# Performance work log

Hardware: AMD Instinct MI355X
Metric: run time of the kernel (lower is better)

Reference implementation:

```python
import jax, jax.numpy as jnp
import numpy as np

N = 10000
E = 160000
D_IN = 512
D_OUT = 512


def setup_inputs() -> dict:
    key = jax.random.key(0)
    k1, k2, k3, k4, k5 = jax.random.split(key, 5)
    x = jax.random.normal(k1, (N, D_IN), dtype=jnp.float32)
    edge_index = jax.random.randint(k2, (2, E), 0, N, dtype=jnp.int64)
    edge_attr = jax.random.uniform(k3, (E,), dtype=jnp.float32)
    W = jax.random.normal(k4, (D_IN, D_OUT), dtype=jnp.float32) * 0.05
    b = jax.random.normal(k5, (D_OUT,), dtype=jnp.float32) * 0.05
    return {"x": x, "edge_index": edge_index, "edge_attr": edge_attr, "W": W, "b": b}


def reference(x, edge_index, edge_attr, W, b):
    # PyG GCNConv with normalize=True, add_self_loops=True, edge_weight=edge_attr.
    n = x.shape[0]
    row, col = edge_index[0], edge_index[1]
    # Add self loops with weight 1.0 (fill_value=1.)
    loop = jnp.arange(n, dtype=edge_index.dtype)
    row_f = jnp.concatenate([row, loop])      # [E+N] source nodes
    col_f = jnp.concatenate([col, loop])      # [E+N] target nodes
    ew = jnp.concatenate([edge_attr, jnp.ones((n,), dtype=edge_attr.dtype)])
    # Symmetric normalization: deg computed over target index (col)
    deg = jax.ops.segment_sum(ew, col_f, num_segments=n)
    dinv = jnp.where(deg > 0, jax.lax.rsqrt(deg), 0.0)
    norm = dinv[row_f] * ew * dinv[col_f]     # [E+N]
    # Linear transform (no bias inside lin), then gather-scale-scatter
    h = x @ W                                  # [N, D_OUT]
    msg = h[row_f] * norm[:, None]             # [E+N, D_OUT]
    out = jax.ops.segment_sum(msg, col_f, num_segments=n)
    return out + b
```

## Files before the change

### kernel.cpp

```cpp
#include <hip/hip_runtime.h>

#define NN 10000
#define EE 160000
#define DD 512
#define CAP 128

typedef float floatx4 __attribute__((ext_vector_type(4)));
typedef short short8 __attribute__((ext_vector_type(8)));

#define AS3(p) ((__attribute__((address_space(3))) void*)(p))
#define AS1(p) ((const __attribute__((address_space(1))) void*)(p))

static __device__ __forceinline__ unsigned short f2bf(float f) {
    unsigned int u = __float_as_uint(f);
    unsigned int r = (u + 0x7fffu + ((u >> 16) & 1u)) >> 16;
    return (unsigned short)r;
}
static __device__ __forceinline__ float bflo(unsigned int u) {
    return __uint_as_float(u << 16);
}
static __device__ __forceinline__ float bfhi(unsigned int u) {
    return __uint_as_float(u & 0xffff0000u);
}


#define XB_BLOCKS 5000
#define WT_BLOCKS 256
#define EDGE_BLOCKS 625

__global__ __launch_bounds__(256) void k_prep(const float* __restrict__ x,
                                              const float* __restrict__ W,
                                              const int* __restrict__ row,
                                              const int* __restrict__ col,
                                              const float* __restrict__ ew,
                                              unsigned short* __restrict__ xb,
                                              unsigned short* __restrict__ wtb,
                                              float* __restrict__ deg,
                                              int* __restrict__ cursor,
                                              uint2* __restrict__ erw) {
    const int b = blockIdx.x;
    const int tid = threadIdx.x;
    if (b < XB_BLOCKS) {
        int gid = b * 256 + tid;
        float4 v = *(const float4*)&x[(size_t)gid * 4];
        unsigned int p0 = (unsigned int)f2bf(v.x) | ((unsigned int)f2bf(v.y) << 16);
        unsigned int p1 = (unsigned int)f2bf(v.z) | ((unsigned int)f2bf(v.w) << 16);
        *(uint2*)&xb[(size_t)gid * 4] = make_uint2(p0, p1);
    } else if (b < XB_BLOCKS + WT_BLOCKS) {
        __shared__ float T[32][33];
        int idx = b - XB_BLOCKS;
        int bi = idx & 15;
        int bj = idx >> 4;
        int r0 = tid >> 5;
        int cc = tid & 31;
        #pragma unroll
        for (int k = 0; k < 4; k++) {
            int r = r0 + k * 8;
            T[r][cc] = W[(size_t)(bi * 32 + r) * DD + bj * 32 + cc];
        }
        __syncthreads();
        #pragma unroll
        for (int k = 0; k < 4; k++) {
            int r = r0 + k * 8;
            wtb[(size_t)(bj * 32 + r) * DD + bi * 32 + cc] = f2bf(T[cc][r]);
        }
    } else {
        int e = (b - XB_BLOCKS - WT_BLOCKS) * 256 + tid;
        int r = row[e];
        int t = col[e];
        float w = ew[e];
        atomicAdd(&deg[t], w);
        int p = atomicAdd(&cursor[t], 1);
        if (p < CAP) erw[t * CAP + p] = make_uint2((unsigned int)r, __float_as_uint(w));
    }
}


__global__ __launch_bounds__(256) void k_gemm_mfma(const unsigned short* __restrict__ xb,
                                                   const unsigned short* __restrict__ wtb,
                                                   const float* __restrict__ deg,
                                                   unsigned short* __restrict__ hb) {
    __shared__ unsigned short As[64 * 32];
    __shared__ unsigned short Bs[128 * 32];

    const int tid = threadIdx.x;
    const int wave = tid >> 6;
    const int lane = tid & 63;

    const int bm = blockIdx.x * 64;
    const int bn = blockIdx.y * 128;

    const int wm = (wave >> 1) * 32;
    const int wn = (wave & 1) * 64;

    const int fm = lane & 15;
    const int kb = (lane >> 4) * 8;

    floatx4 acc[2][4];
    #pragma unroll
    for (int i = 0; i < 2; i++)
        #pragma unroll
        for (int j = 0; j < 4; j++)
            acc[i][j] = (floatx4){0.f, 0.f, 0.f, 0.f};

    const int srow = lane >> 2;
    const int scol = (lane & 3) * 8;

    for (int k0 = 0; k0 < DD; k0 += 32) {
        {
            int r = wave * 16 + srow;
            int gr = bm + r; if (gr > NN - 1) gr = NN - 1;
            __builtin_amdgcn_global_load_lds(AS1(xb + (size_t)gr * DD + k0 + scol),
                                             AS3(&As[wave * 512]), 16, 0, 0);
        }
        #pragma unroll
        for (int cc = 0; cc < 2; cc++) {
            int c = wave + cc * 4;
            int nr = bn + c * 16 + srow;
            __builtin_amdgcn_global_load_lds(AS1(wtb + (size_t)nr * DD + k0 + scol),
                                             AS3(&Bs[c * 512]), 16, 0, 0);
        }
        __syncthreads();

        short8 af[2], bfr[4];
        #pragma unroll
        for (int mi = 0; mi < 2; mi++)
            af[mi] = *(const short8*)&As[(wm + mi * 16 + fm) * 32 + kb];
        #pragma unroll
        for (int ni = 0; ni < 4; ni++)
            bfr[ni] = *(const short8*)&Bs[(wn + ni * 16 + fm) * 32 + kb];

        #pragma unroll
        for (int mi = 0; mi < 2; mi++)
            #pragma unroll
            for (int ni = 0; ni < 4; ni++)
                acc[mi][ni] = __builtin_amdgcn_mfma_f32_16x16x32_bf16(af[mi], bfr[ni], acc[mi][ni], 0, 0, 0);

        __syncthreads();
    }

    float dv[2][4];
    #pragma unroll
    for (int mi = 0; mi < 2; mi++) {
        int rbase = bm + wm + mi * 16 + (lane >> 4) * 4;
        #pragma unroll
        for (int j = 0; j < 4; j++) {
            int rg = rbase + j; if (rg > NN - 1) rg = NN - 1;
            dv[mi][j] = rsqrtf(deg[rg] + 1.0f);
        }
    }

    #pragma unroll
    for (int mi = 0; mi < 2; mi++) {
        #pragma unroll
        for (int ni = 0; ni < 4; ni++) {
            int colg = bn + wn + ni * 16 + (lane & 15);
            int rbase = bm + wm + mi * 16 + (lane >> 4) * 4;
            #pragma unroll
            for (int j = 0; j < 4; j++) {
                int rg = rbase + j;
                if (rg < NN) hb[(size_t)rg * DD + colg] = f2bf(acc[mi][ni][j] * dv[mi][j]);
            }
        }
    }
}


#define EDGE_FMA2(P, W) \
    acc[0] += bflo(P.x) * W; acc[1] += bfhi(P.x) * W; \
    acc[2] += bflo(P.y) * W; acc[3] += bfhi(P.y) * W;

__global__ __launch_bounds__(128, 8) void k_aggregate(const int* __restrict__ cursor,
                                                      const uint2* __restrict__ erw,
                                                      const unsigned short* __restrict__ hb,
                                                      const float* __restrict__ deg,
                                                      const float* __restrict__ bias,
                                                      float* __restrict__ out) {
    const int h = threadIdx.x >> 6;
    const int t = threadIdx.x & 63;
    const int bid = blockIdx.x;
    const int half = bid & 1;
    const int i = (bid >> 1) * 2 + h;
    const int c = half * 256 + t * 4;

    __shared__ int   s_r[2][CAP];
    __shared__ float s_w[2][CAP];

    int cnt = cursor[i];
    if (cnt > CAP) cnt = CAP;
    const uint2* bkt = erw + (size_t)i * CAP;
    if (t < cnt)      { uint2 p = bkt[t];      s_r[h][t]      = (int)p.x; s_w[h][t]      = __uint_as_float(p.y); }
    if (t + 64 < cnt) { uint2 p = bkt[t + 64]; s_r[h][t + 64] = (int)p.x; s_w[h][t + 64] = __uint_as_float(p.y); }

    float dv = rsqrtf(deg[i] + 1.0f);
    uint2 hv = *(const uint2*)&hb[(size_t)i * DD + c];
    float4 bv = *(const float4*)&bias[c];

    __syncthreads();

    float acc[4] = {0.f, 0.f, 0.f, 0.f};

    int j = 0;
    for (; j + 8 <= cnt; j += 8) {
        uint2 p0 = *(const uint2*)&hb[(size_t)s_r[h][j    ] * DD + c];
        uint2 p1 = *(const uint2*)&hb[(size_t)s_r[h][j + 1] * DD + c];
        uint2 p2 = *(const uint2*)&hb[(size_t)s_r[h][j + 2] * DD + c];
        uint2 p3 = *(const uint2*)&hb[(size_t)s_r[h][j + 3] * DD + c];
        uint2 p4 = *(const uint2*)&hb[(size_t)s_r[h][j + 4] * DD + c];
        uint2 p5 = *(const uint2*)&hb[(size_t)s_r[h][j + 5] * DD + c];
        uint2 p6 = *(const uint2*)&hb[(size_t)s_r[h][j + 6] * DD + c];
        uint2 p7 = *(const uint2*)&hb[(size_t)s_r[h][j + 7] * DD + c];
        float w0 = s_w[h][j],     w1 = s_w[h][j + 1], w2 = s_w[h][j + 2], w3 = s_w[h][j + 3];
        float w4 = s_w[h][j + 4], w5 = s_w[h][j + 5], w6 = s_w[h][j + 6], w7 = s_w[h][j + 7];
        EDGE_FMA2(p0, w0) EDGE_FMA2(p1, w1) EDGE_FMA2(p2, w2) EDGE_FMA2(p3, w3)
        EDGE_FMA2(p4, w4) EDGE_FMA2(p5, w5) EDGE_FMA2(p6, w6) EDGE_FMA2(p7, w7)
    }
    for (; j + 4 <= cnt; j += 4) {
        uint2 p0 = *(const uint2*)&hb[(size_t)s_r[h][j    ] * DD + c];
        uint2 p1 = *(const uint2*)&hb[(size_t)s_r[h][j + 1] * DD + c];
        uint2 p2 = *(const uint2*)&hb[(size_t)s_r[h][j + 2] * DD + c];
        uint2 p3 = *(const uint2*)&hb[(size_t)s_r[h][j + 3] * DD + c];
        float w0 = s_w[h][j], w1 = s_w[h][j + 1], w2 = s_w[h][j + 2], w3 = s_w[h][j + 3];
        EDGE_FMA2(p0, w0) EDGE_FMA2(p1, w1) EDGE_FMA2(p2, w2) EDGE_FMA2(p3, w3)
    }
    for (; j < cnt; j++) {
        uint2 p0 = *(const uint2*)&hb[(size_t)s_r[h][j] * DD + c];
        float w0 = s_w[h][j];
        EDGE_FMA2(p0, w0)
    }

    float2 o0, o1;
    o0.x = (acc[0] + bflo(hv.x)) * dv + bv.x;
    o0.y = (acc[1] + bfhi(hv.x)) * dv + bv.y;
    o1.x = (acc[2] + bflo(hv.y)) * dv + bv.z;
    o1.y = (acc[3] + bfhi(hv.y)) * dv + bv.w;
    *(float2*)&out[(size_t)i * DD + c] = o0;
    *(float2*)&out[(size_t)i * DD + c + 2] = o1;
}

extern "C" void kernel_launch(void* const* d_in, const int* in_sizes, int n_in,
                              void* d_out, int out_size, void* d_ws, size_t ws_size,
                              hipStream_t stream) {
    const float* x  = (const float*)d_in[0];
    const int*   ei = (const int*)d_in[1];
    const float* ea = (const float*)d_in[2];
    const float* W  = (const float*)d_in[3];
    const float* b  = (const float*)d_in[4];
    float* out = (float*)d_out;

    char* ws = (char*)d_ws;
    unsigned short* hb   = (unsigned short*)ws;
    unsigned short* xb   = (unsigned short*)(ws + 10240000);
    unsigned short* wtb  = (unsigned short*)(ws + 20480000);
    float* deg    = (float*)(ws + 21004288);
    int*   cursor = (int*)  (ws + 21045248);
    uint2* erw    = (uint2*)(ws + 21086208);

    const int* row = ei;
    const int* col = ei + EE;

    hipMemsetAsync(deg, 0, 81920, stream);

    k_prep<<<XB_BLOCKS + WT_BLOCKS + EDGE_BLOCKS, 256, 0, stream>>>(x, W, row, col, ea,
                                                                    xb, wtb, deg, cursor, erw);

    dim3 ggrid((NN + 63) / 64, DD / 128);
    k_gemm_mfma<<<ggrid, 256, 0, stream>>>(xb, wtb, deg, hb);

    k_aggregate<<<NN, 128, 0, stream>>>(cursor, erw, hb, deg, b, out);
}
```

Measured before the change: 133.0 us.

## Overlap edge bucketing with GEMM and move source-degree scaling to aggregation

The edge bucketing and degree atomics move out of the prep kernel and into the GEMM launch as extra leading blocks, so that scatter work runs alongside the MFMA tiles. Because the GEMM no longer waits for degrees, it stores unscaled h. The aggregation kernel now folds the source dinv into each edge weight, gathering deg[r] per edge, and applies dinv twice for the self-loop term. This removes a dependency between stages at the cost of an extra random deg gather per edge, and h is rounded to bf16 before scaling instead of after.

```diff
diff --git a/kernel.cpp b/kernel.cpp
--- a/kernel.cpp
+++ b/kernel.cpp
@@ -27,17 +27,12 @@
 #define XB_BLOCKS 5000
 #define WT_BLOCKS 256
 #define EDGE_BLOCKS 625
-
-__global__ __launch_bounds__(256) void k_prep(const float* __restrict__ x,
-                                              const float* __restrict__ W,
-                                              const int* __restrict__ row,
-                                              const int* __restrict__ col,
-                                              const float* __restrict__ ew,
-                                              unsigned short* __restrict__ xb,
-                                              unsigned short* __restrict__ wtb,
-                                              float* __restrict__ deg,
-                                              int* __restrict__ cursor,
-                                              uint2* __restrict__ erw) {
+#define GM_BLOCKS (157 * 4)
+
+__global__ __launch_bounds__(256) void k_prep_xw(const float* __restrict__ x,
+                                                 const float* __restrict__ W,
+                                                 unsigned short* __restrict__ xb,
+                                                 unsigned short* __restrict__ wtb) {
     const int b = blockIdx.x;
     const int tid = threadIdx.x;
     if (b < XB_BLOCKS) {
@@ -46,7 +41,7 @@
         unsigned int p0 = (unsigned int)f2bf(v.x) | ((unsigned int)f2bf(v.y) << 16);
         unsigned int p1 = (unsigned int)f2bf(v.z) | ((unsigned int)f2bf(v.w) << 16);
         *(uint2*)&xb[(size_t)gid * 4] = make_uint2(p0, p1);
-    } else if (b < XB_BLOCKS + WT_BLOCKS) {
+    } else {
         __shared__ float T[32][33];
         int idx = b - XB_BLOCKS;
         int bi = idx & 15;
@@ -64,31 +59,41 @@
             int r = r0 + k * 8;
             wtb[(size_t)(bj * 32 + r) * DD + bi * 32 + cc] = f2bf(T[cc][r]);
         }
-    } else {
-        int e = (b - XB_BLOCKS - WT_BLOCKS) * 256 + tid;
+    }
+}
+
+
+__global__ __launch_bounds__(256) void k_gemm_edge(const unsigned short* __restrict__ xb,
+                                                   const unsigned short* __restrict__ wtb,
+                                                   unsigned short* __restrict__ hb,
+                                                   const int* __restrict__ row,
+                                                   const int* __restrict__ col,
+                                                   const float* __restrict__ ew,
+                                                   float* __restrict__ deg,
+                                                   int* __restrict__ cursor,
+                                                   uint2* __restrict__ erw) {
+    __shared__ unsigned short As[64 * 32];
+    __shared__ unsigned short Bs[128 * 32];
+
+    const int tid = threadIdx.x;
+
+    if (blockIdx.x < EDGE_BLOCKS) {
+        int e = blockIdx.x * 256 + tid;
         int r = row[e];
         int t = col[e];
         float w = ew[e];
         atomicAdd(&deg[t], w);
         int p = atomicAdd(&cursor[t], 1);
         if (p < CAP) erw[t * CAP + p] = make_uint2((unsigned int)r, __float_as_uint(w));
-    }
-}
-
-
-__global__ __launch_bounds__(256) void k_gemm_mfma(const unsigned short* __restrict__ xb,
-                                                   const unsigned short* __restrict__ wtb,
-                                                   const float* __restrict__ deg,
-                                                   unsigned short* __restrict__ hb) {
-    __shared__ unsigned short As[64 * 32];
-    __shared__ unsigned short Bs[128 * 32];
-
-    const int tid = threadIdx.x;
+        return;
+    }
+
+    const int bid = blockIdx.x - EDGE_BLOCKS;
     const int wave = tid >> 6;
     const int lane = tid & 63;
 
-    const int bm = blockIdx.x * 64;
-    const int bn = blockIdx.y * 128;
+    const int bm = (bid >> 2) * 64;
+    const int bn = (bid & 3) * 128;
 
     const int wm = (wave >> 1) * 32;
     const int wn = (wave & 1) * 64;
@@ -139,17 +144,6 @@
         __syncthreads();
     }
 
-    float dv[2][4];
-    #pragma unroll
-    for (int mi = 0; mi < 2; mi++) {
-        int rbase = bm + wm + mi * 16 + (lane >> 4) * 4;
-        #pragma unroll
-        for (int j = 0; j < 4; j++) {
-            int rg = rbase + j; if (rg > NN - 1) rg = NN - 1;
-            dv[mi][j] = rsqrtf(deg[rg] + 1.0f);
-        }
-    }
-
     #pragma unroll
     for (int mi = 0; mi < 2; mi++) {
         #pragma unroll
@@ -159,7 +153,7 @@
             #pragma unroll
             for (int j = 0; j < 4; j++) {
                 int rg = rbase + j;
-                if (rg < NN) hb[(size_t)rg * DD + colg] = f2bf(acc[mi][ni][j] * dv[mi][j]);
+                if (rg < NN) hb[(size_t)rg * DD + colg] = f2bf(acc[mi][ni][j]);
             }
         }
     }
@@ -189,8 +183,18 @@
     int cnt = cursor[i];
     if (cnt > CAP) cnt = CAP;
     const uint2* bkt = erw + (size_t)i * CAP;
-    if (t < cnt)      { uint2 p = bkt[t];      s_r[h][t]      = (int)p.x; s_w[h][t]      = __uint_as_float(p.y); }
-    if (t + 64 < cnt) { uint2 p = bkt[t + 64]; s_r[h][t + 64] = (int)p.x; s_w[h][t + 64] = __uint_as_float(p.y); }
+    if (t < cnt) {
+        uint2 p = bkt[t];
+        int r = (int)p.x;
+        s_r[h][t] = r;
+        s_w[h][t] = __uint_as_float(p.y) * rsqrtf(deg[r] + 1.0f);
+    }
+    if (t + 64 < cnt) {
+        uint2 p = bkt[t + 64];
+        int r = (int)p.x;
+        s_r[h][t + 64] = r;
+        s_w[h][t + 64] = __uint_as_float(p.y) * rsqrtf(deg[r] + 1.0f);
+    }
 
     float dv = rsqrtf(deg[i] + 1.0f);
     uint2 hv = *(const uint2*)&hb[(size_t)i * DD + c];
@@ -230,10 +234,10 @@
     }
 
     float2 o0, o1;
-    o0.x = (acc[0] + bflo(hv.x)) * dv + bv.x;
-    o0.y = (acc[1] + bfhi(hv.x)) * dv + bv.y;
-    o1.x = (acc[2] + bflo(hv.y)) * dv + bv.z;
-    o1.y = (acc[3] + bfhi(hv.y)) * dv + bv.w;
+    o0.x = (acc[0] + bflo(hv.x) * dv) * dv + bv.x;
+    o0.y = (acc[1] + bfhi(hv.x) * dv) * dv + bv.y;
+    o1.x = (acc[2] + bflo(hv.y) * dv) * dv + bv.z;
+    o1.y = (acc[3] + bfhi(hv.y) * dv) * dv + bv.w;
     *(float2*)&out[(size_t)i * DD + c] = o0;
     *(float2*)&out[(size_t)i * DD + c + 2] = o1;
 }
@@ -261,11 +265,10 @@
 
     hipMemsetAsync(deg, 0, 81920, stream);
 
-    k_prep<<<XB_BLOCKS + WT_BLOCKS + EDGE_BLOCKS, 256, 0, stream>>>(x, W, row, col, ea,
-                                                                    xb, wtb, deg, cursor, erw);
-
-    dim3 ggrid((NN + 63) / 64, DD / 128);
-    k_gemm_mfma<<<ggrid, 256, 0, stream>>>(xb, wtb, deg, hb);
+    k_prep_xw<<<XB_BLOCKS + WT_BLOCKS, 256, 0, stream>>>(x, W, xb, wtb);
+
+    k_gemm_edge<<<EDGE_BLOCKS + GM_BLOCKS, 256, 0, stream>>>(xb, wtb, hb, row, col, ea,
+                                                             deg, cursor, erw);
 
     k_aggregate<<<NN, 128, 0, stream>>>(cursor, erw, hb, deg, b, out);
 }
```

After: 127.6 us. 4.1% less time.
